# Kernel tuning notes

Measured on AMD Instinct MI355X. Metric: run time of the kernel, lower is better.

The kernel has to match this reference:

```python
import jax, jax.numpy as jnp
import numpy as np

N = 50000      # nodes
E = 800000     # edges (avg degree 16)
IN = 64        # input_dim
OUT = 64       # output_dim
T = 4          # num_node_types
R = 5          # num_relations
H = 4          # heads
D = OUT // H   # head_dim = 16
LN_EPS = 1e-5


def setup_inputs() -> dict:
    key = jax.random.key(0)
    ks = jax.random.split(key, 20)
    s = 0.02
    glorot = np.sqrt(6.0 / (D + D))
    inp = {
        "x": jax.random.normal(ks[0], (N, IN), jnp.float32),
        "node_types": jax.random.randint(ks[1], (N,), 0, T, jnp.int32),
        "edge_index": jax.random.randint(ks[2], (2, E), 0, N, jnp.int64),
        "edge_types": jax.random.randint(ks[3], (E,), 0, R, jnp.int32),
        # per-node-type linear layers, stacked: [T, in, out] / [T, out]
        "Wk": jax.random.normal(ks[4], (T, IN, OUT), jnp.float32) * s,
        "bk": jnp.zeros((T, OUT), jnp.float32),
        "Wq": jax.random.normal(ks[5], (T, IN, OUT), jnp.float32) * s,
        "bq": jnp.zeros((T, OUT), jnp.float32),
        "Wv": jax.random.normal(ks[6], (T, IN, OUT), jnp.float32) * s,
        "bv": jnp.zeros((T, OUT), jnp.float32),
        "Wa": jax.random.normal(ks[7], (T, OUT, OUT), jnp.float32) * s,
        "ba": jnp.zeros((T, OUT), jnp.float32),
        # per-node-type LayerNorm params
        "ln_g": jnp.ones((T, OUT), jnp.float32),
        "ln_b": jnp.zeros((T, OUT), jnp.float32),
        # relation params
        "rel_pri": jnp.ones((R, H), jnp.float32),
        "rel_att": jax.random.uniform(ks[8], (R, H, D, D), jnp.float32, -glorot, glorot),
        "rel_msg": jax.random.uniform(ks[9], (R, H, D, D), jnp.float32, -glorot, glorot),
        "skip_weights": jnp.ones((T,), jnp.float32),
    }
    return inp


def _typed_linear(x, W, b, node_types):
    # per-node-type linear: compute all T projections ([T,N,out] is small: T*N*out)
    # then select each node's row by its type.
    all_t = jnp.einsum('ni,tio->tno', x, W)                       # [T,N,out]
    sel = jnp.take_along_axis(all_t, node_types[None, :, None], axis=0)[0]
    return sel + b[node_types]                                     # [N,out]


def _hgt_forward(x, node_types, edge_index, edge_types,
                 Wk, bk, Wq, bq, Wv, bv, Wa, ba, ln_g, ln_b,
                 rel_pri, rel_att, rel_msg, skip_weights):
    src = edge_index[0]   # j (source)
    tgt = edge_index[1]   # i (target, segment id for softmax / aggregation)

    Kn = _typed_linear(x, Wk, bk, node_types)  # [N,out]
    Qn = _typed_linear(x, Wq, bq, node_types)
    Vn = _typed_linear(x, Wv, bv, node_types)

    q = Qn[tgt].reshape(E, H, D)   # [E,H,D]
    k = Kn[src].reshape(E, H, D)
    v = Vn[src].reshape(E, H, D)

    # relation-specific transforms: k' = k @ rel_att[r], v' = v @ rel_msg[r]
    # loop over the small fixed set of relations (avoids [E,H,D,D] gather)
    k2 = jnp.zeros_like(k)
    v2 = jnp.zeros_like(v)
    for r in range(R):
        m = (edge_types == r)[:, None, None]
        k2 = k2 + jnp.where(m, jnp.einsum('ehd,hdf->ehf', k, rel_att[r]), 0.0)
        v2 = v2 + jnp.where(m, jnp.einsum('ehd,hdf->ehf', v, rel_msg[r]), 0.0)

    scale = np.float32(np.sqrt(D))
    att = (q * k2).sum(-1) * rel_pri[edge_types] / scale           # [E,H]

    # segment softmax over edges sharing a target node
    amax = jax.ops.segment_max(att, tgt, num_segments=N)           # [N,H]
    ex = jnp.exp(att - amax[tgt])
    den = jax.ops.segment_sum(ex, tgt, num_segments=N)             # [N,H]
    attw = ex / den[tgt]                                           # [E,H]

    msg = (v2 * attw[..., None]).reshape(E, OUT)                   # [E,out]
    agg = jax.ops.segment_sum(msg, tgt, num_segments=N)            # [N,out]

    # update: gelu -> per-type linear -> skip mix -> per-type LayerNorm
    # (dropout omitted: eval mode)
    out_g = jax.nn.gelu(agg, approximate=False)
    trans = _typed_linear(out_g, Wa, ba, node_types)               # [N,out]
    sk = jax.nn.sigmoid(skip_weights)[node_types][:, None]         # [N,1]
    res = trans * sk + x * (1.0 - sk)
    mu = res.mean(-1, keepdims=True)
    var = res.var(-1, keepdims=True)
    res = (res - mu) / jnp.sqrt(var + LN_EPS)
    return res * ln_g[node_types] + ln_b[node_types]


def reference(x, node_types, edge_index, edge_types,
              Wk, bk, Wq, bq, Wv, bv, Wa, ba, ln_g, ln_b,
              rel_pri, rel_att, rel_msg, skip_weights):
    return _hgt_forward(x, node_types, edge_index, edge_types,
                        Wk, bk, Wq, bq, Wv, bv, Wa, ba, ln_g, ln_b,
                        rel_pri, rel_att, rel_msg, skip_weights)
```

## Files before the change

### kernel.cpp

```cpp
#include <hip/hip_runtime.h>
#include <math.h>

#define N_NODES 50000
#define N_EDGES 800000

#define OFF_KV     0
#define OFF_QN     3200000
#define OFF_AGG    6400000
#define OFF_RS     9600000
#define OFF_CNT    9660000
#define OFF_PART   10460000
#define OFF_SMALL  10460300
#define OFF_BTH    10460400
#define OFF_ORDER  10461200
#define OFF_COL    10520000

__device__ __forceinline__ float gelu_f(float a) {
    return 0.5f * a * (1.0f + erff(a * 0.70710678118654752f));
}

__device__ __forceinline__ unsigned pack_kv(float kf, float vf) {
    unsigned ku = __float_as_uint(kf);
    ku = (ku + 0x7FFFu + ((ku >> 16) & 1u)) >> 16;
    unsigned vu = __float_as_uint(vf);
    vu = (vu + 0x7FFFu + ((vu >> 16) & 1u)) & 0xFFFF0000u;
    return vu | ku;
}

__global__ __launch_bounds__(256) void hist_k(const int* __restrict__ ei,
                                              const int* __restrict__ ntype,
                                              int* __restrict__ cnt,
                                              int* __restrict__ bth) {
    int e = blockIdx.x * 256 + threadIdx.x;
    atomicAdd(&cnt[ei[N_EDGES + e] << 4], 1);
    if (blockIdx.x < 196) {
        __shared__ int wc[4][4];
        int tid = threadIdx.x, w = tid >> 6, lane = tid & 63;
        int i = blockIdx.x * 256 + tid;
        int t = (i < N_NODES) ? ntype[i] : 255;
#pragma unroll
        for (int tt = 0; tt < 4; ++tt) {
            unsigned long long m = __ballot(t == tt);
            if (lane == 0) wc[w][tt] = __popcll(m);
        }
        __syncthreads();
        if (tid < 4)
            bth[tid * 196 + blockIdx.x] = wc[0][tid] + wc[1][tid] + wc[2][tid] + wc[3][tid];
    }
}

__global__ __launch_bounds__(64) void tscan_k(int* __restrict__ bth,
                                              int* __restrict__ small) {
    __shared__ int tot[4];
    __shared__ int noff_s[4];
    int t = threadIdx.x;
    if (t < 4) {
        int s = 0;
        for (int b = 0; b < 196; ++b) s += bth[t * 196 + b];
        tot[t] = s;
    }
    __syncthreads();
    if (t == 0) {
        int o = 0, cb = 0;
        for (int k = 0; k < 4; ++k) {
            small[k] = tot[k];
            small[8 + k] = o; noff_s[k] = o;
            small[16 + k] = cb;
            o += tot[k]; cb += (tot[k] + 63) >> 6;
        }
        small[12] = o; small[20] = cb;
    }
    __syncthreads();
    if (t < 4) {
        int run = noff_s[t];
        for (int b = 0; b < 196; ++b) {
            int c = bth[t * 196 + b];
            bth[t * 196 + b] = run;
            run += c;
        }
    }
}

__global__ __launch_bounds__(256) void scan1_k(const int* __restrict__ cnt,
                                               int* __restrict__ rs,
                                               int* __restrict__ part) {
    int tid = threadIdx.x;
    int i = blockIdx.x * 256 + tid;
    int lane = tid & 63, w = tid >> 6;
    int c = (i < N_NODES) ? cnt[i << 4] : 0;
    int v = c;
#pragma unroll
    for (int o = 1; o < 64; o <<= 1) { int u = __shfl_up(v, o); if (lane >= o) v += u; }
    __shared__ int wsum[4];
    if (lane == 63) wsum[w] = v;
    __syncthreads();
    int base = 0;
#pragma unroll
    for (int k = 0; k < 4; ++k) if (k < w) base += wsum[k];
    if (i < N_NODES) rs[i] = base + v - c;
    if (tid == 255) part[blockIdx.x] = base + v;
}

__global__ __launch_bounds__(256) void scan2_k(int* __restrict__ part) {
    int tid = threadIdx.x;
    int lane = tid & 63, w = tid >> 6;
    int c = (tid < 196) ? part[tid] : 0;
    int v = c;
#pragma unroll
    for (int o = 1; o < 64; o <<= 1) { int u = __shfl_up(v, o); if (lane >= o) v += u; }
    __shared__ int wsum[4];
    if (lane == 63) wsum[w] = v;
    __syncthreads();
    int base = 0;
#pragma unroll
    for (int k = 0; k < 4; ++k) if (k < w) base += wsum[k];
    if (tid < 196) part[tid] = base + v - c;
}

__global__ __launch_bounds__(256) void scan3_k(int* __restrict__ rs,
                                               const int* __restrict__ part,
                                               const int* __restrict__ ntype,
                                               const int* __restrict__ bth,
                                               int* __restrict__ order) {
    int tid = threadIdx.x, w = tid >> 6, lane = tid & 63;
    int i = blockIdx.x * 256 + tid;
    if (i < N_NODES) rs[i] += part[blockIdx.x];
    if (i == 0) rs[N_NODES] = N_EDGES;
    __shared__ int wc[4][4];
    int t = (i < N_NODES) ? ntype[i] : 255;
    int myrank = 0;
#pragma unroll
    for (int tt = 0; tt < 4; ++tt) {
        unsigned long long m = __ballot(t == tt);
        if (lane == 0) wc[w][tt] = __popcll(m);
        if (t == tt) myrank = __popcll(m & ((1ull << lane) - 1ull));
    }
    __syncthreads();
    if (t < 4) {
        int base = 0;
#pragma unroll
        for (int w2 = 0; w2 < 4; ++w2) if (w2 < w) base += wc[w2][t];
        order[bth[t * 196 + blockIdx.x] + base + myrank] = i;
    }
}

__global__ __launch_bounds__(256) void scatter_col_k(const int* __restrict__ ei,
                                                     const int* __restrict__ et,
                                                     const int* __restrict__ rs,
                                                     int* __restrict__ cnt,
                                                     int* __restrict__ col) {
    int e = blockIdx.x * 256 + threadIdx.x;
    int tgt = ei[N_EDGES + e];
    int old = atomicSub(&cnt[tgt << 4], 1);
    col[rs[tgt] + old - 1] = ei[e] | (et[e] << 20);
}

__device__ __forceinline__ void mat16(const float* __restrict__ W,
                                      const float* __restrict__ B,
                                      const float* xs, int lane, int wvu,
                                      float acc[16]) {
    const float* Bp = B + wvu * 16;
#pragma unroll
    for (int c = 0; c < 16; c += 4) {
        float4 b4 = *(const float4*)(Bp + c);
        acc[c] = b4.x; acc[c + 1] = b4.y; acc[c + 2] = b4.z; acc[c + 3] = b4.w;
    }
    const float* Wp = W + wvu * 16;
#pragma unroll 4
    for (int i = 0; i < 64; ++i) {
        float xi = xs[i * 64 + lane];
#pragma unroll
        for (int c = 0; c < 16; c += 4) {
            float4 w4 = *(const float4*)(Wp + i * 64 + c);
            acc[c]     = fmaf(xi, w4.x, acc[c]);
            acc[c + 1] = fmaf(xi, w4.y, acc[c + 1]);
            acc[c + 2] = fmaf(xi, w4.z, acc[c + 2]);
            acc[c + 3] = fmaf(xi, w4.w, acc[c + 3]);
        }
    }
}

__global__ __launch_bounds__(256) void kqv_k(const float* __restrict__ x,
                                             const int* __restrict__ order,
                                             const int* __restrict__ small,
                                             const float* __restrict__ Wk, const float* __restrict__ bk,
                                             const float* __restrict__ Wq, const float* __restrict__ bq,
                                             const float* __restrict__ Wv, const float* __restrict__ bv,
                                             float* __restrict__ Qn,
                                             unsigned* __restrict__ KVu) {
    __shared__ float xs[4096];
    int tid = threadIdx.x, wv = tid >> 6, lane = tid & 63;
    int wid = blockIdx.x;
    int cb1 = small[17], cb2 = small[18], cb3 = small[19], cb4 = small[20];
    if (wid >= cb4) return;
    int t = (wid >= cb1) + (wid >= cb2) + (wid >= cb3);
    int cbt = small[16 + t];
    int noff = small[8 + t], cntt = small[t];
    int pos = noff + (wid - cbt) * 64 + lane;
    int end = noff + cntt;
    bool valid = pos < end;
    int node = order[valid ? pos : end - 1];
    t = __builtin_amdgcn_readfirstlane(t);
    int wvu = __builtin_amdgcn_readfirstlane(wv);

    const float* xr = x + node * 64 + wvu * 16;
    float4 a0 = *(const float4*)(xr + 0), a1 = *(const float4*)(xr + 4),
           a2 = *(const float4*)(xr + 8), a3 = *(const float4*)(xr + 12);
    float st[16] = { a0.x, a0.y, a0.z, a0.w, a1.x, a1.y, a1.z, a1.w,
                     a2.x, a2.y, a2.z, a2.w, a3.x, a3.y, a3.z, a3.w };
#pragma unroll
    for (int k = 0; k < 16; ++k) xs[(wvu * 16 + k) * 64 + lane] = st[k];
    __syncthreads();

    float aq[16];
    mat16(Wq + t * 4096, bq + t * 64, xs, lane, wvu, aq);
    if (valid) {
        float* Op = Qn + node * 64 + wvu * 16;
#pragma unroll
        for (int c = 0; c < 16; c += 4) {
            float4 o4 = { aq[c], aq[c + 1], aq[c + 2], aq[c + 3] };
            *(float4*)(Op + c) = o4;
        }
    }
    float ak[16], av[16];
    mat16(Wk + t * 4096, bk + t * 64, xs, lane, wvu, ak);
    mat16(Wv + t * 4096, bv + t * 64, xs, lane, wvu, av);
    if (valid) {
        unsigned pk[16];
#pragma unroll
        for (int c = 0; c < 16; ++c) pk[c] = pack_kv(ak[c], av[c]);
        uint4* dst = (uint4*)(KVu + node * 64 + wvu * 16);
#pragma unroll
        for (int c = 0; c < 4; ++c)
            dst[c] = *(uint4*)&pk[c * 4];
    }
}

#define BF_LO(u) __uint_as_float((u) << 16)
#define BF_HI(u) __uint_as_float((u) & 0xFFFF0000u)

#define LOADB(CC, AA, BB, T) do {                                          \
    int idx_ = (T) * 4 + g; if (idx_ > deg - 1) idx_ = deg - 1;            \
    int cc_;                                                               \
    if ((T) < 16) cc_ = __shfl(colv, idx_);                                \
    else          cc_ = col[r0 + idx_];                                    \
    (CC) = cc_;                                                            \
    const unsigned* kvp_ = KVu + (unsigned)(cc_ & 0xFFFFF) * 64;           \
    (AA) = *(const uint2*)(kvp_ + 2 * l);                                  \
    (BB) = *(const uint2*)(kvp_ + 32 + 2 * l);                             \
} while (0)

#define COMPUTE(CC, AA, BB, T) do {                                        \
    int rr_ = (CC) >> 20;                                                  \
    const float* qq_ = qp_s + rr_ * 64 + 2 * l;                            \
    float2 qA_ = *(const float2*)qq_;                                      \
    float2 qB_ = *(const float2*)(qq_ + 32);                               \
    float kA0_ = BF_LO((AA).x), vA0_ = BF_HI((AA).x);                      \
    float kA1_ = BF_LO((AA).y), vA1_ = BF_HI((AA).y);                      \
    float kB0_ = BF_LO((BB).x), vB0_ = BF_HI((BB).x);                      \
    float kB1_ = BF_LO((BB).y), vB1_ = BF_HI((BB).y);                      \
    float sA_ = fmaf(kA1_, qA_.y, kA0_ * qA_.x);                           \
    float sB_ = fmaf(kB1_, qB_.y, kB0_ * qB_.x);                           \
    sA_ += __shfl_xor(sA_, 1); sB_ += __shfl_xor(sB_, 1);                  \
    sA_ += __shfl_xor(sA_, 2); sB_ += __shfl_xor(sB_, 2);                  \
    sA_ += __shfl_xor(sA_, 4); sB_ += __shfl_xor(sB_, 4);                  \
    bool act_ = ((T) * 4 + g) < deg;                                       \
    float pA_ = act_ ? __expf(sA_) : 0.0f;                                 \
    float pB_ = act_ ? __expf(sB_) : 0.0f;                                 \
    dnA += pA_; dnB += pB_;                                                \
    _Pragma("unroll")                                                      \
    for (int k_ = 0; k_ < 5; ++k_) {                                       \
        bool mk_ = (rr_ == k_);                                            \
        float pAk_ = mk_ ? pA_ : 0.0f, pBk_ = mk_ ? pB_ : 0.0f;            \
        OA[k_].x = fmaf(pAk_, vA0_, OA[k_].x);                             \
        OA[k_].y = fmaf(pAk_, vA1_, OA[k_].y);                             \
        OB[k_].x = fmaf(pBk_, vB0_, OB[k_].x);                             \
        OB[k_].y = fmaf(pBk_, vB1_, OB[k_].y);                             \
    }                                                                      \
} while (0)

__global__ __launch_bounds__(256) void attn_k(const float* __restrict__ Qn,
                                              const unsigned* __restrict__ KVu,
                                              const int* __restrict__ rs,
                                              const int* __restrict__ col,
                                              const float* __restrict__ rel_att,
                                              const float* __restrict__ rel_msg,
                                              const float* __restrict__ rel_pri,
                                              float* __restrict__ agg) {
    __shared__ float lds[2816];
    const int tid = threadIdx.x, wv = tid >> 6, lane = tid & 63;
    const int g = lane >> 4, l = lane & 15;
    const int node = blockIdx.x * 4 + wv;
    float* q_s  = lds + wv * 704;
    float* qp_s = q_s + 64;
    float* o_s  = qp_s + 320;

    q_s[lane] = Qn[node * 64 + lane];
    __builtin_amdgcn_wave_barrier();

    const int gb = g * 16;
    float4 qf0 = *(const float4*)(q_s + gb + 0);
    float4 qf1 = *(const float4*)(q_s + gb + 4);
    float4 qf2 = *(const float4*)(q_s + gb + 8);
    float4 qf3 = *(const float4*)(q_s + gb + 12);
#pragma unroll
    for (int r = 0; r < 5; ++r) {
        const float* A = rel_att + ((r * 4 + g) * 16 + l) * 16;
        float4 b0 = *(const float4*)(A + 0), b1 = *(const float4*)(A + 4),
               b2 = *(const float4*)(A + 8), b3 = *(const float4*)(A + 12);
        float acc = b0.x * qf0.x;
        acc = fmaf(b0.y, qf0.y, acc); acc = fmaf(b0.z, qf0.z, acc); acc = fmaf(b0.w, qf0.w, acc);
        acc = fmaf(b1.x, qf1.x, acc); acc = fmaf(b1.y, qf1.y, acc);
        acc = fmaf(b1.z, qf1.z, acc); acc = fmaf(b1.w, qf1.w, acc);
        acc = fmaf(b2.x, qf2.x, acc); acc = fmaf(b2.y, qf2.y, acc);
        acc = fmaf(b2.z, qf2.z, acc); acc = fmaf(b2.w, qf2.w, acc);
        acc = fmaf(b3.x, qf3.x, acc); acc = fmaf(b3.y, qf3.y, acc);
        acc = fmaf(b3.z, qf3.z, acc); acc = fmaf(b3.w, qf3.w, acc);
        qp_s[r * 64 + gb + l] = acc * rel_pri[r * 4 + g] * 0.25f;
    }
    __builtin_amdgcn_wave_barrier();

    int r0 = rs[node], r1 = rs[node + 1];
    int deg = r1 - r0;
    if (deg == 0) {
        agg[node * 64 + lane] = 0.0f;
        return;
    }
    int nit = (deg + 3) >> 2;
    int cidx = r0 + lane;
    int colv = col[(cidx < N_EDGES) ? cidx : (N_EDGES - 1)];

    float dnA = 0.0f, dnB = 0.0f;
    float2 OA[5], OB[5];
#pragma unroll
    for (int k = 0; k < 5; ++k) { OA[k] = {0.f, 0.f}; OB[k] = {0.f, 0.f}; }

    int c0, c1, c2;
    uint2 A0, B0, A1, B1, A2, B2;
    LOADB(c0, A0, B0, 0);
    LOADB(c1, A1, B1, 1);
    LOADB(c2, A2, B2, 2);

    int t = 0;
    for (;;) {
        COMPUTE(c0, A0, B0, t); if (t + 3 < nit) LOADB(c0, A0, B0, t + 3);
        if (++t >= nit) break;
        COMPUTE(c1, A1, B1, t); if (t + 3 < nit) LOADB(c1, A1, B1, t + 3);
        if (++t >= nit) break;
        COMPUTE(c2, A2, B2, t); if (t + 3 < nit) LOADB(c2, A2, B2, t + 3);
        if (++t >= nit) break;
    }

#pragma unroll
    for (int k = 0; k < 5; ++k) {
        OA[k].x += __shfl_xor(OA[k].x, 16); OA[k].x += __shfl_xor(OA[k].x, 32);
        OA[k].y += __shfl_xor(OA[k].y, 16); OA[k].y += __shfl_xor(OA[k].y, 32);
        OB[k].x += __shfl_xor(OB[k].x, 16); OB[k].x += __shfl_xor(OB[k].x, 32);
        OB[k].y += __shfl_xor(OB[k].y, 16); OB[k].y += __shfl_xor(OB[k].y, 32);
    }
    dnA += __shfl_xor(dnA, 16); dnA += __shfl_xor(dnA, 32);
    dnB += __shfl_xor(dnB, 16); dnB += __shfl_xor(dnB, 32);

    if (g == 0) {
#pragma unroll
        for (int k = 0; k < 5; ++k) {
            *(float2*)(o_s + k * 64 + 2 * l) = OA[k];
            *(float2*)(o_s + k * 64 + 32 + 2 * l) = OB[k];
        }
        if (l == 0) { q_s[0] = dnA; q_s[2] = dnB; }
        if (l == 8) { q_s[1] = dnA; q_s[3] = dnB; }
    }
    __builtin_amdgcn_wave_barrier();

    float F = 0.0f;
#pragma unroll
    for (int k = 0; k < 5; ++k) {
        const float* ob = o_s + k * 64 + gb;
        float4 o0 = *(const float4*)(ob + 0), o1 = *(const float4*)(ob + 4),
               o2 = *(const float4*)(ob + 8), o3 = *(const float4*)(ob + 12);
        const float* M = rel_msg + ((k * 4 + g) * 16) * 16 + l;
        F = fmaf(o0.x, M[0],   F); F = fmaf(o0.y, M[16],  F);
        F = fmaf(o0.z, M[32],  F); F = fmaf(o0.w, M[48],  F);
        F = fmaf(o1.x, M[64],  F); F = fmaf(o1.y, M[80],  F);
        F = fmaf(o1.z, M[96],  F); F = fmaf(o1.w, M[112], F);
        F = fmaf(o2.x, M[128], F); F = fmaf(o2.y, M[144], F);
        F = fmaf(o2.z, M[160], F); F = fmaf(o2.w, M[176], F);
        F = fmaf(o3.x, M[192], F); F = fmaf(o3.y, M[208], F);
        F = fmaf(o3.z, M[224], F); F = fmaf(o3.w, M[240], F);
    }
    float dsel = q_s[g];
    float rd = (dsel > 0.0f) ? (1.0f / dsel) : 0.0f;
    agg[node * 64 + lane] = F * rd;
}

__global__ __launch_bounds__(256) void final_k(const float* __restrict__ x,
                                               const int* __restrict__ order,
                                               const int* __restrict__ small,
                                               const float* __restrict__ agg,
                                               const float* __restrict__ Wa,
                                               const float* __restrict__ ba,
                                               const float* __restrict__ ln_g,
                                               const float* __restrict__ ln_b,
                                               const float* __restrict__ skipw,
                                               float* __restrict__ out) {
    __shared__ float xs[4096];
    __shared__ float res_s[4096];
    int tid = threadIdx.x, wv = tid >> 6, lane = tid & 63;
    int wid = blockIdx.x;
    int cb1 = small[17], cb2 = small[18], cb3 = small[19], cb4 = small[20];
    if (wid >= cb4) return;
    int t = (wid >= cb1) + (wid >= cb2) + (wid >= cb3);
    int cbt = small[16 + t];
    int noff = small[8 + t], cntt = small[t];
    int pos = noff + (wid - cbt) * 64 + lane;
    int end = noff + cntt;
    bool valid = pos < end;
    int node = order[valid ? pos : end - 1];
    t = __builtin_amdgcn_readfirstlane(t);
    int wvu = __builtin_amdgcn_readfirstlane(wv);

    const float* ar = agg + node * 64 + wvu * 16;
    float4 a0 = *(const float4*)(ar + 0), a1 = *(const float4*)(ar + 4),
           a2 = *(const float4*)(ar + 8), a3 = *(const float4*)(ar + 12);
    float st[16] = { gelu_f(a0.x), gelu_f(a0.y), gelu_f(a0.z), gelu_f(a0.w),
                     gelu_f(a1.x), gelu_f(a1.y), gelu_f(a1.z), gelu_f(a1.w),
                     gelu_f(a2.x), gelu_f(a2.y), gelu_f(a2.z), gelu_f(a2.w),
                     gelu_f(a3.x), gelu_f(a3.y), gelu_f(a3.z), gelu_f(a3.w) };
#pragma unroll
    for (int k = 0; k < 16; ++k) xs[(wvu * 16 + k) * 64 + lane] = st[k];
    __syncthreads();

    float acc[16];
    const float* Bp = ba + t * 64 + wvu * 16;
#pragma unroll
    for (int c = 0; c < 16; c += 4) {
        float4 b4 = *(const float4*)(Bp + c);
        acc[c] = b4.x; acc[c + 1] = b4.y; acc[c + 2] = b4.z; acc[c + 3] = b4.w;
    }
    const float* Wp = Wa + t * 4096 + wvu * 16;
#pragma unroll 4
    for (int i = 0; i < 64; ++i) {
        float xi = xs[i * 64 + lane];
#pragma unroll
        for (int c = 0; c < 16; c += 4) {
            float4 w4 = *(const float4*)(Wp + i * 64 + c);
            acc[c]     = fmaf(xi, w4.x, acc[c]);
            acc[c + 1] = fmaf(xi, w4.y, acc[c + 1]);
            acc[c + 2] = fmaf(xi, w4.z, acc[c + 2]);
            acc[c + 3] = fmaf(xi, w4.w, acc[c + 3]);
        }
    }
    float sk = 1.0f / (1.0f + __expf(-skipw[t]));
    float om = 1.0f - sk;
    const float* xrow = x + node * 64 + wvu * 16;
#pragma unroll
    for (int c = 0; c < 16; c += 4) {
        float4 xv = *(const float4*)(xrow + c);
        acc[c]     = acc[c] * sk + xv.x * om;
        acc[c + 1] = acc[c + 1] * sk + xv.y * om;
        acc[c + 2] = acc[c + 2] * sk + xv.z * om;
        acc[c + 3] = acc[c + 3] * sk + xv.w * om;
    }
#pragma unroll
    for (int k = 0; k < 16; ++k) res_s[(wvu * 16 + k) * 64 + lane] = acc[k];
    __syncthreads();

    float sum = 0.0f, ssq = 0.0f;
#pragma unroll
    for (int c = 0; c < 64; ++c) {
        float rv = res_s[c * 64 + lane];
        sum += rv; ssq = fmaf(rv, rv, ssq);
    }
    float mu = sum * (1.0f / 64.0f);
    float var = ssq * (1.0f / 64.0f) - mu * mu;
    float rstd = rsqrtf(var + 1e-5f);
    const float* lg = ln_g + t * 64 + wvu * 16;
    const float* lb = ln_b + t * 64 + wvu * 16;
    if (valid) {
        float* op = out + node * 64 + wvu * 16;
#pragma unroll
        for (int c = 0; c < 16; c += 4) {
            float4 ov;
            ov.x = (acc[c]     - mu) * rstd * lg[c]     + lb[c];
            ov.y = (acc[c + 1] - mu) * rstd * lg[c + 1] + lb[c + 1];
            ov.z = (acc[c + 2] - mu) * rstd * lg[c + 2] + lb[c + 2];
            ov.w = (acc[c + 3] - mu) * rstd * lg[c + 3] + lb[c + 3];
            *(float4*)(op + c) = ov;
        }
    }
}

extern "C" void kernel_launch(void* const* d_in, const int* in_sizes, int n_in,
                              void* d_out, int out_size, void* d_ws, size_t ws_size,
                              hipStream_t stream) {
    const float* x       = (const float*)d_in[0];
    const int*   ntype   = (const int*)d_in[1];
    const int*   ei      = (const int*)d_in[2];
    const int*   et      = (const int*)d_in[3];
    const float* Wk      = (const float*)d_in[4];
    const float* bk      = (const float*)d_in[5];
    const float* Wq      = (const float*)d_in[6];
    const float* bq      = (const float*)d_in[7];
    const float* Wv      = (const float*)d_in[8];
    const float* bv      = (const float*)d_in[9];
    const float* Wa      = (const float*)d_in[10];
    const float* ba      = (const float*)d_in[11];
    const float* ln_g    = (const float*)d_in[12];
    const float* ln_b    = (const float*)d_in[13];
    const float* rel_pri = (const float*)d_in[14];
    const float* rel_att = (const float*)d_in[15];
    const float* rel_msg = (const float*)d_in[16];
    const float* skipw   = (const float*)d_in[17];
    float* out = (float*)d_out;

    float* ws = (float*)d_ws;
    unsigned* KVu = (unsigned*)(ws + OFF_KV);
    float* Qn  = ws + OFF_QN;
    float* agg = ws + OFF_AGG;
    int* rs    = (int*)(ws + OFF_RS);
    int* cnt   = (int*)(ws + OFF_CNT);
    int* part  = (int*)(ws + OFF_PART);
    int* small = (int*)(ws + OFF_SMALL);
    int* bth   = (int*)(ws + OFF_BTH);
    int* order = (int*)(ws + OFF_ORDER);
    int* col   = (int*)(ws + OFF_COL);

    hipMemsetAsync(cnt, 0, 800000 * sizeof(int), stream);
    hist_k<<<3125, 256, 0, stream>>>(ei, ntype, cnt, bth);
    tscan_k<<<1, 64, 0, stream>>>(bth, small);
    scan1_k<<<196, 256, 0, stream>>>(cnt, rs, part);
    scan2_k<<<1, 256, 0, stream>>>(part);
    scan3_k<<<196, 256, 0, stream>>>(rs, part, ntype, bth, order);
    scatter_col_k<<<3125, 256, 0, stream>>>(ei, et, rs, cnt, col);
    kqv_k<<<786, 256, 0, stream>>>(x, order, small, Wk, bk, Wq, bq, Wv, bv, Qn, KVu);
    attn_k<<<12500, 256, 0, stream>>>(Qn, KVu, rs, col, rel_att, rel_msg, rel_pri, agg);
    final_k<<<786, 256, 0, stream>>>(x, order, small, agg, Wa, ba, ln_g, ln_b, skipw, out);
}
```

Before: 262.4 us.

## Batch edge gathers four tiles deep and issue them before Q projection

Replaces the three-stage rotating per-tile prefetch in the attention kernel with double-buffered batches of four tiles (up to 32 edges in flight per wave). The row-pointer read and the first two batches of K/V gathers are issued before the relation-specific Q projection, so their latency overlaps that compute. The column index is now read directly from global memory per tile instead of being shuffled from a register preload. This raises register pressure (two buffers of four tiles), which may lower occupancy.

```diff
diff --git a/kernel.cpp b/kernel.cpp
--- a/kernel.cpp
+++ b/kernel.cpp
@@ -239,15 +239,21 @@
 #define BF_LO(u) __uint_as_float((u) << 16)
 #define BF_HI(u) __uint_as_float((u) & 0xFFFF0000u)
 
-#define LOADB(CC, AA, BB, T) do {                                          \
-    int idx_ = (T) * 4 + g; if (idx_ > deg - 1) idx_ = deg - 1;            \
-    int cc_;                                                               \
-    if ((T) < 16) cc_ = __shfl(colv, idx_);                                \
-    else          cc_ = col[r0 + idx_];                                    \
-    (CC) = cc_;                                                            \
-    const unsigned* kvp_ = KVu + (unsigned)(cc_ & 0xFFFFF) * 64;           \
-    (AA) = *(const uint2*)(kvp_ + 2 * l);                                  \
-    (BB) = *(const uint2*)(kvp_ + 32 + 2 * l);                             \
+struct KVB { int cc[4]; uint2 a[4]; uint2 b[4]; };
+
+#define LOAD_BATCH(BUF, BT) do {                                           \
+    _Pragma("unroll")                                                      \
+    for (int tt_ = 0; tt_ < 4; ++tt_) {                                    \
+        int tile_ = (BT) * 4 + tt_;                                        \
+        if (tile_ < nit) {                                                 \
+            int idx_ = tile_ * 4 + g; if (idx_ > deg - 1) idx_ = deg - 1;  \
+            int cc_ = col[r0 + idx_];                                      \
+            BUF.cc[tt_] = cc_;                                             \
+            const unsigned* kvp_ = KVu + (unsigned)(cc_ & 0xFFFFF) * 64;   \
+            BUF.a[tt_] = *(const uint2*)(kvp_ + 2 * l);                    \
+            BUF.b[tt_] = *(const uint2*)(kvp_ + 32 + 2 * l);               \
+        }                                                                  \
+    }                                                                      \
 } while (0)
 
 #define COMPUTE(CC, AA, BB, T) do {                                        \
@@ -279,6 +285,15 @@
     }                                                                      \
 } while (0)
 
+#define COMPUTE_BATCH(BUF, BT) do {                                        \
+    _Pragma("unroll")                                                      \
+    for (int tt_c = 0; tt_c < 4; ++tt_c) {                                 \
+        int tile_c = (BT) * 4 + tt_c;                                      \
+        if (tile_c < nit)                                                  \
+            COMPUTE(BUF.cc[tt_c], BUF.a[tt_c], BUF.b[tt_c], tile_c);       \
+    }                                                                      \
+} while (0)
+
 __global__ __launch_bounds__(256) void attn_k(const float* __restrict__ Qn,
                                               const unsigned* __restrict__ KVu,
                                               const int* __restrict__ rs,
@@ -295,9 +310,27 @@
     float* qp_s = q_s + 64;
     float* o_s  = qp_s + 320;
 
-    q_s[lane] = Qn[node * 64 + lane];
+    int r0 = rs[node], r1 = rs[node + 1];
+    float qv = Qn[node * 64 + lane];
+    int deg = r1 - r0;
+    if (deg == 0) {
+        agg[node * 64 + lane] = 0.0f;
+        return;
+    }
+    int nit = (deg + 3) >> 2;
+    int nb = (nit + 3) >> 2;
+
+    float dnA = 0.0f, dnB = 0.0f;
+    float2 OA[5], OB[5];
+#pragma unroll
+    for (int k = 0; k < 5; ++k) { OA[k] = {0.f, 0.f}; OB[k] = {0.f, 0.f}; }
+
+    KVB X0, X1;
+    LOAD_BATCH(X0, 0);
+    if (nb > 1) LOAD_BATCH(X1, 1);
+
+    q_s[lane] = qv;
     __builtin_amdgcn_wave_barrier();
-
     const int gb = g * 16;
     float4 qf0 = *(const float4*)(q_s + gb + 0);
     float4 qf1 = *(const float4*)(q_s + gb + 4);
@@ -320,35 +353,14 @@
     }
     __builtin_amdgcn_wave_barrier();
 
-    int r0 = rs[node], r1 = rs[node + 1];
-    int deg = r1 - r0;
-    if (deg == 0) {
-        agg[node * 64 + lane] = 0.0f;
-        return;
-    }
-    int nit = (deg + 3) >> 2;
-    int cidx = r0 + lane;
-    int colv = col[(cidx < N_EDGES) ? cidx : (N_EDGES - 1)];
-
-    float dnA = 0.0f, dnB = 0.0f;
-    float2 OA[5], OB[5];
-#pragma unroll
-    for (int k = 0; k < 5; ++k) { OA[k] = {0.f, 0.f}; OB[k] = {0.f, 0.f}; }
-
-    int c0, c1, c2;
-    uint2 A0, B0, A1, B1, A2, B2;
-    LOADB(c0, A0, B0, 0);
-    LOADB(c1, A1, B1, 1);
-    LOADB(c2, A2, B2, 2);
-
-    int t = 0;
+    int b = 0;
     for (;;) {
-        COMPUTE(c0, A0, B0, t); if (t + 3 < nit) LOADB(c0, A0, B0, t + 3);
-        if (++t >= nit) break;
-        COMPUTE(c1, A1, B1, t); if (t + 3 < nit) LOADB(c1, A1, B1, t + 3);
-        if (++t >= nit) break;
-        COMPUTE(c2, A2, B2, t); if (t + 3 < nit) LOADB(c2, A2, B2, t + 3);
-        if (++t >= nit) break;
+        COMPUTE_BATCH(X0, b);
+        if (++b >= nb) break;
+        if (b + 1 < nb) LOAD_BATCH(X0, b + 1);
+        COMPUTE_BATCH(X1, b);
+        if (++b >= nb) break;
+        if (b + 1 < nb) LOAD_BATCH(X1, b + 1);
     }
 
 #pragma unroll
```

Result: no change. 260.9 us (-0.6%).
